# Kernel optimization log

Measured on AMD Instinct MI355X. Metric: run time of the kernel, lower is better.

Reference implementation:

```python
import jax, jax.numpy as jnp
import numpy as np

N = 50000   # nodes
E = 800000  # edges
H = 64      # hidden channels
EPS = 1e-16  # PyG softmax denominator epsilon


def _ptconv(x, pos, src, dst, W_src, W_dst, W_val, W_pos, b_pos):
    """PyG PointTransformerConv: per-edge gather, positional MLP, vector
    attention (segment softmax over edges grouped by dst), scatter-sum.
    edge_index convention: src = j (neighbor), dst = i (center)."""
    a_src = x @ W_src          # [N,H] alpha_j projection
    a_dst = x @ W_dst          # [N,H] alpha_i projection
    v = x @ W_val              # [N,H] values
    # relative positional encoding: pos_nn(pos_i - pos_j), [E,H]
    delta = (pos[dst] - pos[src]) @ W_pos + b_pos
    alpha = a_dst[dst] - a_src[src] + delta           # [E,H]
    # numerically-stable vector softmax over variable-size neighborhoods
    m = jax.lax.stop_gradient(jax.ops.segment_max(alpha, dst, num_segments=N))
    e = jnp.exp(alpha - m[dst])
    s = jax.ops.segment_sum(e, dst, num_segments=N)
    attn = e / (s[dst] + EPS)                         # [E,H]
    return jax.ops.segment_sum(attn * (v[src] + delta), dst, num_segments=N)


def setup_inputs() -> dict:
    key = jax.random.key(0)
    ks = jax.random.split(key, 16)
    x = jax.random.normal(ks[0], (N, 3), dtype=jnp.float32)
    pos = jax.random.normal(ks[1], (N, 3), dtype=jnp.float32)
    edge_index = jax.random.randint(ks[2], (2, E), 0, N)
    batch = jnp.zeros((N,), dtype=jnp.int32)

    def lin(k, i, o):
        return (jax.random.normal(k, (i, o), dtype=jnp.float32)
                * np.float32(1.0 / np.sqrt(i)))

    return {
        "x": x, "pos": pos, "edge_index": edge_index, "batch": batch,
        # conv1 (in=3 -> H)
        "W1_src": lin(ks[3], 3, H), "W1_dst": lin(ks[4], 3, H),
        "W1_val": lin(ks[5], 3, H),
        "W1_pos": lin(ks[6], 3, H), "b1_pos": jnp.zeros((H,), jnp.float32),
        # conv2 (H -> H)
        "W2_src": lin(ks[7], H, H), "W2_dst": lin(ks[8], H, H),
        "W2_val": lin(ks[9], H, H),
        "W2_pos": lin(ks[10], 3, H), "b2_pos": jnp.zeros((H,), jnp.float32),
        # MLP head
        "W_fc1": lin(ks[11], H, H // 2), "b_fc1": jnp.zeros((H // 2,), jnp.float32),
        "W_fc2": lin(ks[12], H // 2, 1), "b_fc2": jnp.zeros((1,), jnp.float32),
    }


def reference(x, pos, edge_index, batch,
              W1_src, W1_dst, W1_val, W1_pos, b1_pos,
              W2_src, W2_dst, W2_val, W2_pos, b2_pos,
              W_fc1, b_fc1, W_fc2, b_fc2):
    src, dst = edge_index[0], edge_index[1]
    h = jax.nn.relu(_ptconv(x, pos, src, dst, W1_src, W1_dst, W1_val, W1_pos, b1_pos))
    h = jax.nn.relu(_ptconv(h, pos, src, dst, W2_src, W2_dst, W2_val, W2_pos, b2_pos))
    h = jax.nn.relu(h @ W_fc1 + b_fc1)
    return h @ W_fc2 + b_fc2  # [N, 1]
```

## Files before the change

### kernel.cpp

```cpp
#include <hip/hip_runtime.h>
#include <hip/hip_fp16.h>
#include <math.h>


#define LOG2E 1.44269504088896340736f

typedef _Float16 hf2 __attribute__((ext_vector_type(2)));
union H2U { __half2 hh; hf2 hf; unsigned u; };

#if defined(__has_builtin)
#if __has_builtin(__builtin_amdgcn_fdot2)
#define HAVE_FDOT2 1
#endif
#endif

__device__ __forceinline__ float fdot2(hf2 a, hf2 b, float c) {
#ifdef HAVE_FDOT2
    return __builtin_amdgcn_fdot2(a, b, c, false);
#else
    return fmaf((float)a.x, (float)b.x, fmaf((float)a.y, (float)b.y, c));
#endif
}

__device__ __forceinline__ unsigned bf16_rn(float x) {
    unsigned b = __float_as_uint(x);
    return (b + 0x7FFFu + ((b >> 16) & 1u)) >> 16;
}

__device__ __forceinline__ unsigned pack_payload(float a_plus_c, float vv) {
    float t = fminf(fmaxf(-a_plus_c * LOG2E, -86.0f), 86.0f);
    float E = exp2f(t);
    return (bf16_rn(E) << 16) | bf16_rn(E * vv);
}

__global__ void __launch_bounds__(256) hist_proj1_kernel(
        const int* __restrict__ dst, int* __restrict__ count8, int* __restrict__ rank,
        const float* __restrict__ x, const float* __restrict__ pos,
        const float* __restrict__ W1_src, const float* __restrict__ W1_val,
        const float* __restrict__ W1_pos,
        unsigned* __restrict__ g1, int N, int E) {
    int gtid = blockIdx.x * 256 + threadIdx.x;
    int gsz = gridDim.x * 256;
    int* cnt = count8 + (blockIdx.x & 7) * N;
    for (int e = gtid; e < E; e += gsz)
        rank[e] = atomicAdd(&cnt[dst[e]], 1);

    int lane = threadIdx.x & 63, wid = threadIdx.x >> 6;
    float ws0 = W1_src[lane], ws1 = W1_src[64 + lane], ws2 = W1_src[128 + lane];
    float wv0 = W1_val[lane], wv1 = W1_val[64 + lane], wv2 = W1_val[128 + lane];
    float wp0 = W1_pos[lane], wp1 = W1_pos[64 + lane], wp2 = W1_pos[128 + lane];
    int nwav = gridDim.x * 4;
    for (int node = blockIdx.x * 4 + wid; node < N; node += nwav) {
        float x0 = x[node * 3 + 0], x1 = x[node * 3 + 1], x2 = x[node * 3 + 2];
        float p0 = pos[node * 3 + 0], p1 = pos[node * 3 + 1], p2 = pos[node * 3 + 2];
        float as = fmaf(x0, ws0, fmaf(x1, ws1, x2 * ws2));
        float vv = fmaf(x0, wv0, fmaf(x1, wv1, x2 * wv2));
        float cc = fmaf(p0, wp0, fmaf(p1, wp1, p2 * wp2));
        g1[node * 64 + lane] = pack_payload(as + cc, vv - cc);
    }
}

__global__ void __launch_bounds__(256) scan_kernel(
        const int* __restrict__ count8, int* __restrict__ offsets,
        int* __restrict__ base8, int n, int nsb) {
    __shared__ int red[4];
    __shared__ int wpre[4];
    int tid = threadIdx.x, lane = tid & 63, wid = tid >> 6;
    int lim = blockIdx.x * 1024;
    int s = 0;
    #pragma unroll
    for (int j = 0; j < 8; ++j) {
        const int* cj = count8 + j * n;
        for (int i = tid * 4; i < lim; i += 1024) {
            int4 c = *(const int4*)&cj[i];
            s += c.x + c.y + c.z + c.w;
        }
    }
    #pragma unroll
    for (int off = 32; off >= 1; off >>= 1) s += __shfl_down(s, off);
    if (lane == 0) red[wid] = s;
    __syncthreads();
    int base = red[0] + red[1] + red[2] + red[3];

    int b4 = lim + tid * 4;
    int c[8][4];
    #pragma unroll
    for (int j = 0; j < 8; ++j) {
        int4 v = make_int4(0, 0, 0, 0);
        if (b4 + 3 < n) {
            v = *(const int4*)&count8[j * n + b4];
        } else {
            if (b4 + 0 < n) v.x = count8[j * n + b4 + 0];
            if (b4 + 1 < n) v.y = count8[j * n + b4 + 1];
            if (b4 + 2 < n) v.z = count8[j * n + b4 + 2];
        }
        c[j][0] = v.x; c[j][1] = v.y; c[j][2] = v.z; c[j][3] = v.w;
    }
    int tot[4];
    #pragma unroll
    for (int k = 0; k < 4; ++k) {
        tot[k] = 0;
        #pragma unroll
        for (int j = 0; j < 8; ++j) tot[k] += c[j][k];
    }
    int tsum = tot[0] + tot[1] + tot[2] + tot[3];
    int inc = tsum;
    #pragma unroll
    for (int off = 1; off < 64; off <<= 1) {
        int t2 = __shfl_up(inc, off);
        if (lane >= off) inc += t2;
    }
    if (lane == 63) wpre[wid] = inc;
    __syncthreads();
    int wbase = 0;
    for (int q = 0; q < wid; ++q) wbase += wpre[q];
    int run = base + wbase + (inc - tsum);
    #pragma unroll
    for (int k = 0; k < 4; ++k) {
        int i = b4 + k;
        if (i < n) {
            offsets[i] = run;
            int pb = run;
            #pragma unroll
            for (int j = 0; j < 8; ++j) {
                base8[j * n + i] = pb;
                pb += c[j][k];
            }
            run += tot[k];
        }
    }
    if ((int)blockIdx.x == nsb - 1 && tid == 0)
        offsets[n] = base + wpre[0] + wpre[1] + wpre[2] + wpre[3];
}

__global__ void __launch_bounds__(256) scatter_kernel(
        const int* __restrict__ src, const int* __restrict__ dst,
        const int* __restrict__ rank, const int* __restrict__ base8,
        int* __restrict__ sorted_src, int N, int E) {
    int gtid = blockIdx.x * 256 + threadIdx.x;
    int gsz = gridDim.x * 256;
    const int* bj = base8 + (blockIdx.x & 7) * N;
    for (int e = gtid; e < E; e += gsz)
        sorted_src[bj[dst[e]] + rank[e]] = src[e];
}

__device__ __forceinline__ void eacc(unsigned u, float& s, float& n) {
    s += __uint_as_float(u & 0xFFFF0000u);
    n += __uint_as_float(u << 16);
}

__device__ __forceinline__ float edge_node(
        int node, int laneoff,
        const int* __restrict__ offsets, const int* __restrict__ ss,
        const char* __restrict__ gbase, float dv) {
    int beg = offsets[node], end = offsets[node + 1];
    if (beg >= end) return 0.f;
    float s0 = 0.f, n0 = 0.f, s1 = 0.f, n1 = 0.f;
    int e = beg;
    int aligned = min((beg + 3) & ~3, end);
    for (; e < aligned; ++e) {
        int i0 = __builtin_amdgcn_readfirstlane(ss[e]);
        unsigned g0 = *(const unsigned*)(gbase + (((size_t)(unsigned)i0) << 8) + laneoff);
        eacc(g0, s0, n0);
    }
    for (; e + 8 <= end; e += 8) {
        int4 ia = *(const int4*)(ss + e);
        int4 ib = *(const int4*)(ss + e + 4);
        int i0 = __builtin_amdgcn_readfirstlane(ia.x);
        int i1 = __builtin_amdgcn_readfirstlane(ia.y);
        int i2 = __builtin_amdgcn_readfirstlane(ia.z);
        int i3 = __builtin_amdgcn_readfirstlane(ia.w);
        int i4 = __builtin_amdgcn_readfirstlane(ib.x);
        int i5 = __builtin_amdgcn_readfirstlane(ib.y);
        int i6 = __builtin_amdgcn_readfirstlane(ib.z);
        int i7 = __builtin_amdgcn_readfirstlane(ib.w);
        unsigned g0 = *(const unsigned*)(gbase + (((size_t)(unsigned)i0) << 8) + laneoff);
        unsigned g1 = *(const unsigned*)(gbase + (((size_t)(unsigned)i1) << 8) + laneoff);
        unsigned g2 = *(const unsigned*)(gbase + (((size_t)(unsigned)i2) << 8) + laneoff);
        unsigned g3 = *(const unsigned*)(gbase + (((size_t)(unsigned)i3) << 8) + laneoff);
        unsigned g4 = *(const unsigned*)(gbase + (((size_t)(unsigned)i4) << 8) + laneoff);
        unsigned g5 = *(const unsigned*)(gbase + (((size_t)(unsigned)i5) << 8) + laneoff);
        unsigned g6 = *(const unsigned*)(gbase + (((size_t)(unsigned)i6) << 8) + laneoff);
        unsigned g7 = *(const unsigned*)(gbase + (((size_t)(unsigned)i7) << 8) + laneoff);
        eacc(g0, s0, n0);
        eacc(g1, s1, n1);
        eacc(g2, s0, n0);
        eacc(g3, s1, n1);
        eacc(g4, s0, n0);
        eacc(g5, s1, n1);
        eacc(g6, s0, n0);
        eacc(g7, s1, n1);
    }
    for (; e + 4 <= end; e += 4) {
        int4 ia = *(const int4*)(ss + e);
        int i0 = __builtin_amdgcn_readfirstlane(ia.x);
        int i1 = __builtin_amdgcn_readfirstlane(ia.y);
        int i2 = __builtin_amdgcn_readfirstlane(ia.z);
        int i3 = __builtin_amdgcn_readfirstlane(ia.w);
        unsigned g0 = *(const unsigned*)(gbase + (((size_t)(unsigned)i0) << 8) + laneoff);
        unsigned g1 = *(const unsigned*)(gbase + (((size_t)(unsigned)i1) << 8) + laneoff);
        unsigned g2 = *(const unsigned*)(gbase + (((size_t)(unsigned)i2) << 8) + laneoff);
        unsigned g3 = *(const unsigned*)(gbase + (((size_t)(unsigned)i3) << 8) + laneoff);
        eacc(g0, s0, n0);
        eacc(g1, s1, n1);
        eacc(g2, s0, n0);
        eacc(g3, s1, n1);
    }
    for (; e < end; ++e) {
        int i0 = __builtin_amdgcn_readfirstlane(ss[e]);
        unsigned g0 = *(const unsigned*)(gbase + (((size_t)(unsigned)i0) << 8) + laneoff);
        eacc(g0, s0, n0);
    }
    float s = s0 + s1;
    float r = __builtin_amdgcn_rcpf(s + 1e-37f);
    return fmaxf(fmaf(n0 + n1, r, dv), 0.f);
}

__global__ void __launch_bounds__(256, 8) e1p2_kernel(
        const float* __restrict__ pos,
        const int* __restrict__ offsets, const int* __restrict__ sorted_src,
        const unsigned* __restrict__ g1,
        const float* __restrict__ W1_pos, const float* __restrict__ b1_pos,
        const float* __restrict__ W2_src, const float* __restrict__ W2_val,
        const float* __restrict__ W2_pos,
        unsigned* __restrict__ g2, int N) {
    __shared__ uint4 W4q[16 * 64];
    __shared__ __half hsh[4][64];
    int tid = threadIdx.x, lane = tid & 63, wid = tid >> 6;
    for (int idx = tid; idx < 1024; idx += 256) {
        int q = idx >> 6, c = idx & 63, k = 4 * q;
        H2U s01, s23, v01, v23;
        s01.hh = __floats2half2_rn(W2_src[k * 64 + c], W2_src[(k + 1) * 64 + c]);
        s23.hh = __floats2half2_rn(W2_src[(k + 2) * 64 + c], W2_src[(k + 3) * 64 + c]);
        v01.hh = __floats2half2_rn(W2_val[k * 64 + c], W2_val[(k + 1) * 64 + c]);
        v23.hh = __floats2half2_rn(W2_val[(k + 2) * 64 + c], W2_val[(k + 3) * 64 + c]);
        W4q[idx] = make_uint4(s01.u, s23.u, v01.u, v23.u);
    }
    __syncthreads();

    float w1p0 = W1_pos[lane], w1p1 = W1_pos[64 + lane], w1p2 = W1_pos[128 + lane];
    float bp1 = b1_pos[lane];
    float w2p0 = W2_pos[lane], w2p1 = W2_pos[64 + lane], w2p2 = W2_pos[128 + lane];
    int laneoff = lane * 4;
    int nwav = gridDim.x * 4;

    for (int node = blockIdx.x * 4 + wid; node < N; node += nwav) {
        float p0 = pos[node * 3 + 0], p1 = pos[node * 3 + 1], p2 = pos[node * 3 + 2];
        float dpos = fmaf(p0, w1p0, fmaf(p1, w1p1, p2 * w1p2));
        float hval = edge_node(node, laneoff, offsets, sorted_src,
                               (const char*)g1, dpos + bp1);
        hsh[wid][lane] = __float2half(hval);
        const uint2* hq = (const uint2*)hsh[wid];
        float as = 0.f, vv = 0.f;
        #pragma unroll 4
        for (int q = 0; q < 16; ++q) {
            uint2 hu = hq[q];
            H2U h01, h23; h01.u = hu.x; h23.u = hu.y;
            uint4 wq = W4q[q * 64 + lane];
            H2U a0, a1, b0, b1;
            a0.u = wq.x; a1.u = wq.y; b0.u = wq.z; b1.u = wq.w;
            as = fdot2(h01.hf, a0.hf, as);
            as = fdot2(h23.hf, a1.hf, as);
            vv = fdot2(h01.hf, b0.hf, vv);
            vv = fdot2(h23.hf, b1.hf, vv);
        }
        float cc = fmaf(p0, w2p0, fmaf(p1, w2p1, p2 * w2p2));
        g2[node * 64 + lane] = pack_payload(as + cc, vv - cc);
    }
}

__global__ void __launch_bounds__(256, 8) e2head_kernel(
        const float* __restrict__ pos,
        const int* __restrict__ offsets, const int* __restrict__ sorted_src,
        const unsigned* __restrict__ g2,
        const float* __restrict__ W2_pos, const float* __restrict__ b2_pos,
        const float* __restrict__ Wfc1, const float* __restrict__ bfc1,
        const float* __restrict__ Wfc2, const float* __restrict__ bfc2,
        float* __restrict__ out, int N) {
    __shared__ __half hsh[4][64];
    int tid = threadIdx.x, lane = tid & 63, wid = tid >> 6;
    int c = lane & 31, khb = (lane >> 5) * 16;
    unsigned Wr[16];
    #pragma unroll
    for (int j = 0; j < 16; ++j) {
        H2U w;
        w.hh = __floats2half2_rn(Wfc1[(2 * (khb + j)) * 32 + c],
                                 Wfc1[(2 * (khb + j) + 1) * 32 + c]);
        Wr[j] = w.u;
    }

    float wp0 = W2_pos[lane], wp1 = W2_pos[64 + lane], wp2 = W2_pos[128 + lane];
    float bp = b2_pos[lane];
    float bfc1c = bfc1[c], wfc2c = Wfc2[c], bias2 = bfc2[0];
    int laneoff = lane * 4;
    int nwav = gridDim.x * 4;

    for (int node = blockIdx.x * 4 + wid; node < N; node += nwav) {
        float p0 = pos[node * 3 + 0], p1 = pos[node * 3 + 1], p2 = pos[node * 3 + 2];
        float dpos = fmaf(p0, wp0, fmaf(p1, wp1, p2 * wp2));
        float hval = edge_node(node, laneoff, offsets, sorted_src,
                               (const char*)g2, dpos + bp);
        hsh[wid][lane] = __float2half(hval);
        const hf2* h2 = (const hf2*)hsh[wid];
        float t2 = 0.f;
        #pragma unroll
        for (int j = 0; j < 16; ++j) {
            hf2 hk = h2[khb + j];
            H2U w; w.u = Wr[j];
            t2 = fdot2(hk, w.hf, t2);
        }
        t2 += __shfl_down(t2, 32);
        t2 = fmaxf(t2 + bfc1c, 0.f) * wfc2c;
        t2 = (lane < 32) ? t2 : 0.f;
        #pragma unroll
        for (int off = 16; off >= 1; off >>= 1) t2 += __shfl_down(t2, off);
        if (lane == 0) out[node] = t2 + bias2;
    }
}

extern "C" void kernel_launch(void* const* d_in, const int* in_sizes, int n_in,
                              void* d_out, int out_size, void* d_ws, size_t ws_size,
                              hipStream_t stream) {
    const float* x   = (const float*)d_in[0];
    const float* pos = (const float*)d_in[1];
    const int* eidx  = (const int*)d_in[2];
    const float* W1_src = (const float*)d_in[4];
    const float* W1_val = (const float*)d_in[6];
    const float* W1_pos = (const float*)d_in[7];
    const float* b1_pos = (const float*)d_in[8];
    const float* W2_src = (const float*)d_in[9];
    const float* W2_val = (const float*)d_in[11];
    const float* W2_pos = (const float*)d_in[12];
    const float* b2_pos = (const float*)d_in[13];
    const float* W_fc1  = (const float*)d_in[14];
    const float* b_fc1  = (const float*)d_in[15];
    const float* W_fc2  = (const float*)d_in[16];
    const float* b_fc2  = (const float*)d_in[17];

    const int N = in_sizes[0] / 3;
    const int E = in_sizes[2] / 2;
    const int* src = eidx;
    const int* dst = eidx + E;
    const int nsb = (N + 1023) / 1024;

    char* w = (char*)d_ws;
    auto carve = [&](size_t bytes) -> void* {
        void* p = (void*)w;
        w += (bytes + 255) & ~size_t(255);
        return p;
    };
    int*      count8     = (int*)carve((size_t)8 * N * 4);
    int*      offsets    = (int*)carve((size_t)(N + 1) * 4);
    int*      base8      = (int*)carve((size_t)8 * N * 4);
    int*      rank       = (int*)carve((size_t)E * 4);
    int*      sorted_src = (int*)carve((size_t)E * 4);
    unsigned* g1         = (unsigned*)carve((size_t)N * 64 * 4);
    unsigned* g2         = (unsigned*)carve((size_t)N * 64 * 4);

    hipMemsetAsync(count8, 0, (size_t)8 * N * 4, stream);
    hist_proj1_kernel<<<2048, 256, 0, stream>>>(
        dst, count8, rank, x, pos, W1_src, W1_val, W1_pos, g1, N, E);
    scan_kernel<<<nsb, 256, 0, stream>>>(count8, offsets, base8, N, nsb);
    scatter_kernel<<<2048, 256, 0, stream>>>(src, dst, rank, base8,
                                             sorted_src, N, E);
    e1p2_kernel<<<2048, 256, 0, stream>>>(
        pos, offsets, sorted_src, g1, W1_pos, b1_pos, W2_src, W2_val, W2_pos, g2, N);
    e2head_kernel<<<2048, 256, 0, stream>>>(
        pos, offsets, sorted_src, g2, W2_pos, b2_pos,
        W_fc1, b_fc1, W_fc2, b_fc2, (float*)d_out, N);
}
```

Baseline: 258.3 us.

## Split prefix scan into chunk-sum and emit kernels to avoid quadratic rereads

The single scan kernel had each block re-sum all preceding counts, so total work grew quadratically with block count. It is replaced by a reduce-then-scan pair: one kernel writes per-chunk sums, and a second scans those sums within one wavefront and emits the offsets and per-slice bases. This adds an extra kernel launch and assumes at most 64 chunks (N up to 65536).

```diff
diff --git a/kernel.cpp b/kernel.cpp
--- a/kernel.cpp
+++ b/kernel.cpp
@@ -60,30 +60,12 @@
     }
 }
 
-__global__ void __launch_bounds__(256) scan_kernel(
-        const int* __restrict__ count8, int* __restrict__ offsets,
-        int* __restrict__ base8, int n, int nsb) {
+__global__ void __launch_bounds__(256) scan_sum_kernel(
+        const int* __restrict__ count8, int* __restrict__ chunksum, int n) {
     __shared__ int red[4];
-    __shared__ int wpre[4];
     int tid = threadIdx.x, lane = tid & 63, wid = tid >> 6;
-    int lim = blockIdx.x * 1024;
+    int b4 = blockIdx.x * 1024 + tid * 4;
     int s = 0;
-    #pragma unroll
-    for (int j = 0; j < 8; ++j) {
-        const int* cj = count8 + j * n;
-        for (int i = tid * 4; i < lim; i += 1024) {
-            int4 c = *(const int4*)&cj[i];
-            s += c.x + c.y + c.z + c.w;
-        }
-    }
-    #pragma unroll
-    for (int off = 32; off >= 1; off >>= 1) s += __shfl_down(s, off);
-    if (lane == 0) red[wid] = s;
-    __syncthreads();
-    int base = red[0] + red[1] + red[2] + red[3];
-
-    int b4 = lim + tid * 4;
-    int c[8][4];
     #pragma unroll
     for (int j = 0; j < 8; ++j) {
         int4 v = make_int4(0, 0, 0, 0);
@@ -94,6 +76,45 @@
             if (b4 + 1 < n) v.y = count8[j * n + b4 + 1];
             if (b4 + 2 < n) v.z = count8[j * n + b4 + 2];
         }
+        s += v.x + v.y + v.z + v.w;
+    }
+    #pragma unroll
+    for (int off = 32; off >= 1; off >>= 1) s += __shfl_down(s, off);
+    if (lane == 0) red[wid] = s;
+    __syncthreads();
+    if (tid == 0) chunksum[blockIdx.x] = red[0] + red[1] + red[2] + red[3];
+}
+
+__global__ void __launch_bounds__(256) scan_emit_kernel(
+        const int* __restrict__ count8, const int* __restrict__ chunksum,
+        int* __restrict__ offsets, int* __restrict__ base8, int n, int nsb) {
+    __shared__ int sbase[2];
+    __shared__ int wpre[4];
+    int tid = threadIdx.x, lane = tid & 63, wid = tid >> 6;
+    if (tid < 64) {
+        int v = (lane < nsb) ? chunksum[lane] : 0;
+        int inc = v;
+        #pragma unroll
+        for (int off = 1; off < 64; off <<= 1) {
+            int t2 = __shfl_up(inc, off);
+            if (lane >= off) inc += t2;
+        }
+        if (lane == (int)blockIdx.x) sbase[0] = inc - v;
+        if (lane == nsb - 1) sbase[1] = inc;
+    }
+
+    int b4 = blockIdx.x * 1024 + tid * 4;
+    int c[8][4];
+    #pragma unroll
+    for (int j = 0; j < 8; ++j) {
+        int4 v = make_int4(0, 0, 0, 0);
+        if (b4 + 3 < n) {
+            v = *(const int4*)&count8[j * n + b4];
+        } else {
+            if (b4 + 0 < n) v.x = count8[j * n + b4 + 0];
+            if (b4 + 1 < n) v.y = count8[j * n + b4 + 1];
+            if (b4 + 2 < n) v.z = count8[j * n + b4 + 2];
+        }
         c[j][0] = v.x; c[j][1] = v.y; c[j][2] = v.z; c[j][3] = v.w;
     }
     int tot[4];
@@ -114,7 +135,7 @@
     __syncthreads();
     int wbase = 0;
     for (int q = 0; q < wid; ++q) wbase += wpre[q];
-    int run = base + wbase + (inc - tsum);
+    int run = sbase[0] + wbase + (inc - tsum);
     #pragma unroll
     for (int k = 0; k < 4; ++k) {
         int i = b4 + k;
@@ -129,8 +150,7 @@
             run += tot[k];
         }
     }
-    if ((int)blockIdx.x == nsb - 1 && tid == 0)
-        offsets[n] = base + wpre[0] + wpre[1] + wpre[2] + wpre[3];
+    if (blockIdx.x == 0 && tid == 0) offsets[n] = sbase[1];
 }
 
 __global__ void __launch_bounds__(256) scatter_kernel(
@@ -352,6 +372,7 @@
     int*      count8     = (int*)carve((size_t)8 * N * 4);
     int*      offsets    = (int*)carve((size_t)(N + 1) * 4);
     int*      base8      = (int*)carve((size_t)8 * N * 4);
+    int*      chunksum   = (int*)carve((size_t)64 * 4);
     int*      rank       = (int*)carve((size_t)E * 4);
     int*      sorted_src = (int*)carve((size_t)E * 4);
     unsigned* g1         = (unsigned*)carve((size_t)N * 64 * 4);
@@ -360,7 +381,9 @@
     hipMemsetAsync(count8, 0, (size_t)8 * N * 4, stream);
     hist_proj1_kernel<<<2048, 256, 0, stream>>>(
         dst, count8, rank, x, pos, W1_src, W1_val, W1_pos, g1, N, E);
-    scan_kernel<<<nsb, 256, 0, stream>>>(count8, offsets, base8, N, nsb);
+    scan_sum_kernel<<<nsb, 256, 0, stream>>>(count8, chunksum, N);
+    scan_emit_kernel<<<nsb, 256, 0, stream>>>(count8, chunksum, offsets, base8,
+                                              N, nsb);
     scatter_kernel<<<2048, 256, 0, stream>>>(src, dst, rank, base8,
                                              sorted_src, N, E);
     e1p2_kernel<<<2048, 256, 0, stream>>>(
```

Result: faster. 225.9 us (-12.6%).
